# Kernel optimization log

Measured on AMD Instinct MI355X. Metric: run time of the kernel, lower is better.

Reference implementation:

```python
import jax, jax.numpy as jnp
import numpy as np

DIM = 128
HEADS = 4
POS_DIM = (DIM // 4) // 4  # DynamicPosBias: pos_dim = (dim//4)//4 = 8


def _layernorm(x, g, b, eps=1e-5):
    m = x.mean(-1, keepdims=True)
    v = x.var(-1, keepdims=True)
    return (x - m) / jnp.sqrt(v + eps) * g + b


def setup_inputs() -> dict:
    key = jax.random.key(0)
    ks = jax.random.split(key, 16)
    B_, N, C = 64, 512, DIM
    s = 0.02
    inp = {
        "x": jax.random.normal(ks[0], (B_, N, C), jnp.float32),
        "y": jax.random.normal(ks[1], (B_, N, C), jnp.float32),
        "H": 8, "W": 8, "D": 8,
        "qkv_w": jax.random.normal(ks[2], (3 * C, C), jnp.float32) * s,
        "qkv_b": jnp.zeros((3 * C,), jnp.float32),
        "proj_w": jax.random.normal(ks[3], (C, C), jnp.float32) * s,
        "proj_b": jnp.zeros((C,), jnp.float32),
        "pos_proj_w": jax.random.normal(ks[4], (POS_DIM, 3), jnp.float32) * s,
        "pos_proj_b": jnp.zeros((POS_DIM,), jnp.float32),
        "ln1_g": jnp.ones((POS_DIM,), jnp.float32),
        "ln1_b": jnp.zeros((POS_DIM,), jnp.float32),
        "p1_w": jax.random.normal(ks[5], (POS_DIM, POS_DIM), jnp.float32) * s,
        "p1_b": jnp.zeros((POS_DIM,), jnp.float32),
        "ln2_g": jnp.ones((POS_DIM,), jnp.float32),
        "ln2_b": jnp.zeros((POS_DIM,), jnp.float32),
        "p2_w": jax.random.normal(ks[6], (POS_DIM, POS_DIM), jnp.float32) * s,
        "p2_b": jnp.zeros((POS_DIM,), jnp.float32),
        "ln3_g": jnp.ones((POS_DIM,), jnp.float32),
        "ln3_b": jnp.zeros((POS_DIM,), jnp.float32),
        "p3_w": jax.random.normal(ks[7], (HEADS, POS_DIM), jnp.float32) * s,
        "p3_b": jnp.zeros((HEADS,), jnp.float32),
    }
    return inp


def _rel_pos_static(H, W, D):
    # biases table: all relative offsets, shape ((2H-1)(2W-1)(2D-1), 3)
    bh = np.arange(1 - H, H)
    bw = np.arange(1 - W, W)
    bd = np.arange(1 - D, D)
    biases = np.stack(np.meshgrid(bh, bw, bd, indexing="ij")).reshape(3, -1).T
    # relative position index, shape (N, N)
    coords = np.stack(np.meshgrid(np.arange(H), np.arange(W), np.arange(D), indexing="ij")).reshape(3, -1)
    rel = coords[:, :, None] - coords[:, None, :]  # (3, N, N)
    rel = rel.transpose(1, 2, 0).astype(np.int64)
    rel[:, :, 0] += H - 1
    rel[:, :, 1] += W - 1
    rel[:, :, 2] += D - 1
    rel[:, :, 0] *= (2 * W - 1) * (2 * D - 1)
    rel[:, :, 1] *= 2 * D - 1
    idx = rel.sum(-1)  # (N, N)
    return jnp.asarray(biases, jnp.float32), jnp.asarray(idx)


def reference(x, y, H, W, D, qkv_w, qkv_b, proj_w, proj_b,
              pos_proj_w, pos_proj_b, ln1_g, ln1_b, p1_w, p1_b,
              ln2_g, ln2_b, p2_w, p2_b, ln3_g, ln3_b, p3_w, p3_b):
    B_, N, C = x.shape
    h = p3_b.shape[0]
    hd = C // h
    scale = hd ** -0.5

    def qkv_fn(t):
        q3 = (t @ qkv_w.T + qkv_b).reshape(B_, N, 3, h, hd)
        q3 = q3.transpose(2, 0, 3, 1, 4)  # (3, B, h, N, hd)
        return q3[0], q3[1], q3[2]

    q, k, v = qkv_fn(x)
    # NOTE: original code uses self.qkv(y) (not qkv_y) -- reproduced faithfully
    q_y, k_y, v_y = qkv_fn(y)

    attn = jnp.einsum("bhnd,bhmd->bhnm", q * scale, k_y)  # (B, h, N, N)

    biases, idx = _rel_pos_static(H, W, D)
    # DynamicPosBias, residual=False: pos3(pos2(pos1(pos_proj(b))))
    pos = biases @ pos_proj_w.T + pos_proj_b
    pos = jax.nn.relu(_layernorm(pos, ln1_g, ln1_b)) @ p1_w.T + p1_b
    pos = jax.nn.relu(_layernorm(pos, ln2_g, ln2_b)) @ p2_w.T + p2_b
    pos = jax.nn.relu(_layernorm(pos, ln3_g, ln3_b)) @ p3_w.T + p3_b  # (table, h)
    rpb = pos[idx.reshape(-1)].reshape(N, N, h).transpose(2, 0, 1)  # (h, N, N)

    attn = jax.nn.softmax(attn + rpb[None], axis=-1)
    out = jnp.einsum("bhnm,bhmd->bhnd", attn, v_y)
    out = out.transpose(0, 2, 1, 3).reshape(B_, N, C)
    out = out @ proj_w.T + proj_b
    return out
```

## Files before the change

### kernel.cpp

```cpp
#include <hip/hip_runtime.h>
#include <hip/hip_bf16.h>

typedef __attribute__((ext_vector_type(4))) float f32x4;
typedef __attribute__((ext_vector_type(8))) short bf16x8;
typedef __attribute__((ext_vector_type(4))) short bf16x4;
typedef __attribute__((ext_vector_type(2))) unsigned int u32x2;

#define DEV static __device__ __forceinline__

constexpr float LOG2E  = 1.4426950408889634f;
constexpr float QSCALE = 0.17677669529663687f * LOG2E;

constexpr size_t OFF_Q   = 0;
constexpr size_t OFF_K   = (size_t)8  << 20;
constexpr size_t OFF_V   = (size_t)16 << 20;
constexpr size_t OFF_RPB = (size_t)24 << 20;
constexpr size_t OFF_AO  = (size_t)27 << 20;
constexpr size_t OFF_POS = (size_t)35 << 20;
constexpr size_t OFF_WQ  = (size_t)36 << 20;
constexpr size_t OFF_WP  = (size_t)37 << 20;

DEV short f2b(float f) {
  union { __bf16 h; short s; } u;
  u.h = (__bf16)f;
  return u.s;
}
DEV float b2f(unsigned int u) {
  union { unsigned int u; float f; } x; x.u = u; return x.f;
}
DEV unsigned int pkbf(float a, float b) {
  union { __bf16 h; unsigned short s; } ua, ub;
  ua.h = (__bf16)a; ub.h = (__bf16)b;
  return (unsigned int)ua.s | ((unsigned int)ub.s << 16);
}

DEV void ln_relu8(const float* v, const float* __restrict__ g,
                  const float* __restrict__ b, float* t) {
  float m = 0.f;
#pragma unroll
  for (int i = 0; i < 8; i++) m += v[i];
  m *= 0.125f;
  float var = 0.f;
#pragma unroll
  for (int i = 0; i < 8; i++) { float d = v[i] - m; var += d * d; }
  var *= 0.125f;
  float inv = 1.0f / sqrtf(var + 1e-5f);
#pragma unroll
  for (int i = 0; i < 8; i++) {
    float u = (v[i] - m) * inv * g[i] + b[i];
    t[i] = u > 0.f ? u : 0.f;
  }
}

DEV void mm8(const float* t, const float* __restrict__ w,
             const float* __restrict__ c, float* o) {
#pragma unroll
  for (int oo = 0; oo < 8; oo++) {
    float a = c[oo];
#pragma unroll
    for (int i = 0; i < 8; i++) a += t[i] * w[oo * 8 + i];
    o[oo] = a;
  }
}

__global__ void ca_setup(
    const float* __restrict__ qkv_w, const float* __restrict__ proj_w,
    short* __restrict__ wq, short* __restrict__ wp,
    const float* __restrict__ pw, const float* __restrict__ pb,
    const float* __restrict__ g1, const float* __restrict__ b1,
    const float* __restrict__ w1, const float* __restrict__ c1,
    const float* __restrict__ g2, const float* __restrict__ b2,
    const float* __restrict__ w2, const float* __restrict__ c2,
    const float* __restrict__ g3, const float* __restrict__ b3,
    const float* __restrict__ w3, const float* __restrict__ c3,
    float* __restrict__ pos_out) {
  const int blk = blockIdx.x;
  if (blk < 256) {
    int i = blk * 256 + threadIdx.x;
    if (i < 49152) {
      float f = qkv_w[i];
      if (i < 16384) f *= QSCALE;
      wq[i] = f2b(f);
    } else {
      int j = i - 49152;
      wp[j] = f2b(proj_w[j]);
    }
    return;
  }
  int r = (blk - 256) * 256 + threadIdx.x;
  if (r >= 3375) return;
  float x0 = (float)(r / 225 - 7);
  float x1 = (float)((r / 15) % 15 - 7);
  float x2 = (float)(r % 15 - 7);
  float v[8], t[8], u[8];
#pragma unroll
  for (int o = 0; o < 8; o++)
    v[o] = x0 * pw[o * 3] + x1 * pw[o * 3 + 1] + x2 * pw[o * 3 + 2] + pb[o];
  ln_relu8(v, g1, b1, t);
  mm8(t, w1, c1, u);
  ln_relu8(u, g2, b2, t);
  mm8(t, w2, c2, v);
  ln_relu8(v, g3, b3, t);
#pragma unroll
  for (int hh = 0; hh < 4; hh++) {
    float a = c3[hh];
#pragma unroll
    for (int i = 0; i < 8; i++) a += t[i] * w3[hh * 8 + i];
    pos_out[r * 4 + hh] = a * LOG2E;
  }
}

__global__ void ca_rpb(const float* __restrict__ pos, short* __restrict__ rpbf) {
  int gid = blockIdx.x * 256 + threadIdx.x;
  int lane = gid & 63, jc = (gid >> 6) & 31, qg = (gid >> 11) & 31, hh = gid >> 16;
  int q = qg * 16 + (lane & 15);
  int j0 = jc * 16 + (lane >> 4) * 4;
  bf16x4 outv;
#pragma unroll
  for (int r = 0; r < 4; r++) {
    int j = j0 + r;
    int rh = (q >> 6) - (j >> 6) + 7;
    int rw = ((q >> 3) & 7) - ((j >> 3) & 7) + 7;
    int rd = (q & 7) - (j & 7) + 7;
    int idx = (rh * 15 + rw) * 15 + rd;
    outv[r] = f2b(pos[idx * 4 + hh]);
  }
  *(bf16x4*)(rpbf + (size_t)gid * 4) = outv;
}

__global__ __launch_bounds__(256) void ca_qkv(
    const float* __restrict__ x, const float* __restrict__ y,
    const short* __restrict__ wq, const float* __restrict__ qkv_b,
    short* __restrict__ gq, short* __restrict__ gk, short* __restrict__ gv) {
  __shared__ short lds[16384];
  const int z = blockIdx.y;
  const int t0 = blockIdx.x * 64;
  const int b_ = t0 >> 9;
  const int n0 = t0 & 511;
  const int tid = threadIdx.x;
  const float* __restrict__ in = (z == 0) ? x : y;
#pragma unroll
  for (int i = 0; i < 8; i++) {
    int flat = i * 1024 + tid * 4;
    f32x4 f = *(const f32x4*)(in + (size_t)t0 * 128 + flat);
    int row = flat >> 7, col = flat & 127;
    bf16x4 hv;
#pragma unroll
    for (int e = 0; e < 4; e++) hv[e] = f2b(f[e]);
    *(bf16x4*)(lds + row * 136 + col) = hv;
  }
  __syncthreads();
  const int w = tid >> 6, lane = tid & 63, lr = lane & 15, lg = lane >> 4;
  bf16x8 afrag[4];
  {
    const short* ap = lds + (w * 16 + lr) * 136 + lg * 8;
#pragma unroll
    for (int k4 = 0; k4 < 4; k4++) afrag[k4] = *(const bf16x8*)(ap + k4 * 32);
  }
  __syncthreads();

  const int nct = z ? 16 : 8;
  for (int ct = 0; ct < nct; ct++) {
    const int col = z * 128 + ct * 16;
    float bias = qkv_b[col + lr];
    if (z == 0) bias *= QSCALE;
    f32x4 acc = {bias, bias, bias, bias};
    const short* bp = wq + (size_t)(col + lr) * 128 + lg * 8;
#pragma unroll
    for (int k4 = 0; k4 < 4; k4++) {
      bf16x8 bfr = *(const bf16x8*)(bp + k4 * 32);
      acc = __builtin_amdgcn_mfma_f32_16x16x32_bf16(afrag[k4], bfr, acc, 0, 0, 0);
    }
    if (z == 1 && ct >= 8) {
      const int hv_ = (ct - 8) >> 1;
      const int dh = (ct - 8) & 1;
      const int base = 8192 + (((hv_ * 2 + (w >> 1)) * 2 + dh) * 512) + lane * 8 + (w & 1) * 4;
      *(unsigned int*)(lds + base)     = pkbf(acc[0], acc[1]);
      *(unsigned int*)(lds + base + 2) = pkbf(acc[2], acc[3]);
    } else {
      const int d = (ct & 1) * 16 + lr;
      const int base = (w * 4 + (ct >> 1)) * 512 + 128 * (d >> 3) + (d & 7);
#pragma unroll
      for (int r = 0; r < 4; r++)
        lds[base + (lg * 4 + r) * 8] = f2b(acc[r]);
    }
  }
  __syncthreads();
  if (z == 0) {
#pragma unroll
    for (int kk = 0; kk < 4; kk++) {
      const int c = kk * 4 + w, hh = c & 3, tg = c >> 2;
      bf16x8 vd = *(const bf16x8*)(lds + c * 512 + lane * 8);
      *(bf16x8*)(gq + (((size_t)b_ * 4 + hh) * 32 + (n0 >> 4) + tg) * 512 + lane * 8) = vd;
    }
  } else {
#pragma unroll
    for (int kk = 0; kk < 4; kk++) {
      const int c = kk * 4 + w, hh = c & 3, tg = c >> 2;
      bf16x8 vd = *(const bf16x8*)(lds + c * 512 + lane * 8);
      *(bf16x8*)(gk + (((size_t)b_ * 4 + hh) * 32 + (n0 >> 4) + tg) * 512 + lane * 8) = vd;
    }
#pragma unroll
    for (int kk = 0; kk < 4; kk++) {
      const int c = kk * 4 + w, hh = c >> 2, ul = (c >> 1) & 1, dh = c & 1;
      bf16x8 vd = *(const bf16x8*)(lds + 8192 + c * 512 + lane * 8);
      *(bf16x8*)(gv + ((((size_t)b_ * 4 + hh) * 16 + (n0 >> 5) + ul) * 2 + dh) * 512 + lane * 8) = vd;
    }
  }
}

DEV void stage_kv(const short* kg, const short* vg, short* buf, int T, int w, int lane) {
#pragma unroll
  for (int i = 0; i < 4; i++) {
    const int c = w * 4 + i;
    const short* src;
    short* dst;
    if (c < 8) {
      src = kg + ((size_t)(T * 8 + c)) * 512 + lane * 8;
      dst = buf + c * 512;
    } else {
      src = vg + ((size_t)(T * 8 + c - 8)) * 512 + lane * 8;
      dst = buf + 4096 + (c - 8) * 512;
    }
    __builtin_amdgcn_global_load_lds((const __attribute__((address_space(1))) void*)src,
                                     (__attribute__((address_space(3))) void*)dst, 16, 0, 0);
  }
}

__global__ __launch_bounds__(256, 4) void ca_attn(
    const short* __restrict__ qfrag, const short* __restrict__ kfrag,
    const short* __restrict__ vfrag, const short* __restrict__ rpbf,
    short* __restrict__ aob) {
  __shared__ short kv[2][8192];
  const int bid = blockIdx.x;
  const int qt = bid >> 8, rem = bid & 255;
  const int b_ = rem >> 2, hh = rem & 3;
  const int bh = b_ * 4 + hh;
  const int tid = threadIdx.x;
  const int w = tid >> 6, lane = tid & 63, lg = lane >> 4;
  const int q0 = qt * 64 + w * 16, qg = (q0 >> 4);

  const short* kg = kfrag + (size_t)bh * 16384;
  const short* vg = vfrag + (size_t)bh * 16384;
  const bf16x8 qf = *(const bf16x8*)(qfrag + ((size_t)bh * 32 + qg) * 512 + lane * 8);
  const short* bp = rpbf + ((size_t)(hh * 32 + qg) << 13) + lane * 4;

  union PU { bf16x8 v; unsigned int u[4]; };
  PU ones;
  ones.u[0] = 0x3F803F80u; ones.u[1] = 0x3F803F80u;
  ones.u[2] = 0x3F803F80u; ones.u[3] = 0x3F803F80u;

  stage_kv(kg, vg, &kv[0][0], 0, w, lane);
  __syncthreads();

  f32x4 o0 = {0.f, 0.f, 0.f, 0.f}, o1 = {0.f, 0.f, 0.f, 0.f}, o2 = {0.f, 0.f, 0.f, 0.f};

  for (int T = 0; T < 4; T++) {
    const int cur = T & 1;
    if (T < 3) stage_kv(kg, vg, &kv[cur ^ 1][0], T + 1, w, lane);
    const short* kt = &kv[cur][0];
    const short* vt = &kv[cur][4096];

    u32x2 bw[8];
#pragma unroll
    for (int t = 0; t < 8; t++) bw[t] = *(const u32x2*)(bp + (size_t)(T * 8 + t) * 256);

#pragma unroll
    for (int uu = 0; uu < 4; uu++) {
      PU p;
#pragma unroll
      for (int half = 0; half < 2; half++) {
        const int t = uu * 2 + half;
        bf16x8 kf = *(const bf16x8*)(kt + t * 512 + lane * 8);
        f32x4 cin;
        cin[0] = b2f(bw[t].x << 16);
        cin[1] = b2f(bw[t].x & 0xFFFF0000u);
        cin[2] = b2f(bw[t].y << 16);
        cin[3] = b2f(bw[t].y & 0xFFFF0000u);
        f32x4 s = __builtin_amdgcn_mfma_f32_16x16x32_bf16(kf, qf, cin, 0, 0, 0);
        p.u[half * 2 + 0] = pkbf(__builtin_exp2f(s[0]), __builtin_exp2f(s[1]));
        p.u[half * 2 + 1] = pkbf(__builtin_exp2f(s[2]), __builtin_exp2f(s[3]));
      }
      bf16x8 vf0 = *(const bf16x8*)(vt + (uu * 2 + 0) * 512 + lane * 8);
      bf16x8 vf1 = *(const bf16x8*)(vt + (uu * 2 + 1) * 512 + lane * 8);
      o0 = __builtin_amdgcn_mfma_f32_16x16x32_bf16(p.v, vf0, o0, 0, 0, 0);
      o1 = __builtin_amdgcn_mfma_f32_16x16x32_bf16(p.v, vf1, o1, 0, 0, 0);
      o2 = __builtin_amdgcn_mfma_f32_16x16x32_bf16(p.v, ones.v, o2, 0, 0, 0);
    }
    if (T < 3) __syncthreads();
  }

  short* pt = &kv[0][w * 1024];
  const int lr = lane & 15;
#pragma unroll
  for (int r = 0; r < 4; r++) {
    float iv = 1.0f / o2[r];
    pt[(lg * 4 + r) * 40 + lr] = f2b(o0[r] * iv);
    pt[(lg * 4 + r) * 40 + 16 + lr] = f2b(o1[r] * iv);
  }
  asm volatile("s_waitcnt lgkmcnt(0)" ::: "memory");
  __builtin_amdgcn_sched_barrier(0);
  {
    const int qq = lane >> 2, pp = lane & 3;
    bf16x8 od = *(const bf16x8*)(pt + qq * 40 + pp * 8);
    *(bf16x8*)(aob + ((size_t)bh * 512 + q0 + qq) * 32 + pp * 8) = od;
  }
}

__global__ __launch_bounds__(256) void ca_proj(
    const short* __restrict__ aob, const short* __restrict__ wp,
    const float* __restrict__ proj_b, float* __restrict__ out) {
  const int t0 = blockIdx.x * 64;
  const int b_ = t0 >> 9, n0 = t0 & 511;
  const int tid = threadIdx.x;
  const int w = tid >> 6, lane = tid & 63, lr = lane & 15, lg = lane >> 4;
  bf16x8 afrag[4];
#pragma unroll
  for (int k4 = 0; k4 < 4; k4++)
    afrag[k4] = *(const bf16x8*)(aob + (((size_t)b_ * 4 + k4) * 512 + n0 + w * 16 + lr) * 32 + lg * 8);
#pragma unroll
  for (int ct = 0; ct < 8; ct++) {
    float bias = proj_b[ct * 16 + lr];
    f32x4 acc = {bias, bias, bias, bias};
    const short* bp = wp + (size_t)(ct * 16 + lr) * 128 + lg * 8;
#pragma unroll
    for (int k4 = 0; k4 < 4; k4++) {
      bf16x8 bfr = *(const bf16x8*)(bp + k4 * 32);
      acc = __builtin_amdgcn_mfma_f32_16x16x32_bf16(afrag[k4], bfr, acc, 0, 0, 0);
    }
#pragma unroll
    for (int r = 0; r < 4; r++)
      out[(size_t)(t0 + w * 16 + lg * 4 + r) * 128 + ct * 16 + lr] = acc[r];
  }
}

extern "C" void kernel_launch(void* const* d_in, const int* in_sizes, int n_in,
                              void* d_out, int out_size, void* d_ws, size_t ws_size,
                              hipStream_t stream) {
  const float* x      = (const float*)d_in[0];
  const float* y      = (const float*)d_in[1];
  const float* qkv_w  = (const float*)d_in[5];
  const float* qkv_b  = (const float*)d_in[6];
  const float* proj_w = (const float*)d_in[7];
  const float* proj_b = (const float*)d_in[8];
  const float* pos_w  = (const float*)d_in[9];
  const float* pos_b  = (const float*)d_in[10];
  const float* ln1g = (const float*)d_in[11];
  const float* ln1b = (const float*)d_in[12];
  const float* p1w  = (const float*)d_in[13];
  const float* p1b  = (const float*)d_in[14];
  const float* ln2g = (const float*)d_in[15];
  const float* ln2b = (const float*)d_in[16];
  const float* p2w  = (const float*)d_in[17];
  const float* p2b  = (const float*)d_in[18];
  const float* ln3g = (const float*)d_in[19];
  const float* ln3b = (const float*)d_in[20];
  const float* p3w  = (const float*)d_in[21];
  const float* p3b  = (const float*)d_in[22];
  float* out = (float*)d_out;

  char* ws = (char*)d_ws;
  short* gq    = (short*)(ws + OFF_Q);
  short* gk    = (short*)(ws + OFF_K);
  short* gv    = (short*)(ws + OFF_V);
  short* rpbf  = (short*)(ws + OFF_RPB);
  short* aob   = (short*)(ws + OFF_AO);
  float* posb  = (float*)(ws + OFF_POS);
  short* wq    = (short*)(ws + OFF_WQ);
  short* wp    = (short*)(ws + OFF_WP);

  ca_setup<<<270, 256, 0, stream>>>(qkv_w, proj_w, wq, wp,
                                    pos_w, pos_b, ln1g, ln1b, p1w, p1b,
                                    ln2g, ln2b, p2w, p2b, ln3g, ln3b, p3w, p3b, posb);
  ca_rpb<<<1024, 256, 0, stream>>>(posb, rpbf);
  ca_qkv<<<dim3(512, 2), 256, 0, stream>>>(x, y, wq, qkv_b, gq, gk, gv);
  ca_attn<<<2048, 256, 0, stream>>>(gq, gk, gv, rpbf, aob);
  ca_proj<<<512, 256, 0, stream>>>(aob, wp, proj_b, out);
}
```

Measured before the change: 84.36 us.

## Fuse pos-bias setup with RPB gather, widen blocks, stage full K/V once

Merges the pos-bias MLP and relative-position-bias gather into one kernel that keeps each head's table in LDS, dropping one launch and a global round trip. QKV, attention and projection kernels move to 512-thread blocks covering 128 tokens. Attention now loads all of K/V for a (batch, head) into LDS once instead of double-buffering four tiles, and raises wave priority around the PV MFMAs. The projection output is staged through LDS so the fp32 global stores are coalesced. These changes trade a larger LDS footprint per block for fewer launches and fewer barriers, which may lower occupancy.

```diff
diff --git a/kernel.cpp b/kernel.cpp
--- a/kernel.cpp
+++ b/kernel.cpp
@@ -16,7 +16,6 @@
 constexpr size_t OFF_V   = (size_t)16 << 20;
 constexpr size_t OFF_RPB = (size_t)24 << 20;
 constexpr size_t OFF_AO  = (size_t)27 << 20;
-constexpr size_t OFF_POS = (size_t)35 << 20;
 constexpr size_t OFF_WQ  = (size_t)36 << 20;
 constexpr size_t OFF_WP  = (size_t)37 << 20;
 
@@ -63,85 +62,84 @@
   }
 }
 
-__global__ void ca_setup(
+__global__ void ca_pre(
     const float* __restrict__ qkv_w, const float* __restrict__ proj_w,
     short* __restrict__ wq, short* __restrict__ wp,
+    short* __restrict__ rpbf,
     const float* __restrict__ pw, const float* __restrict__ pb,
     const float* __restrict__ g1, const float* __restrict__ b1,
     const float* __restrict__ w1, const float* __restrict__ c1,
     const float* __restrict__ g2, const float* __restrict__ b2,
     const float* __restrict__ w2, const float* __restrict__ c2,
     const float* __restrict__ g3, const float* __restrict__ b3,
-    const float* __restrict__ w3, const float* __restrict__ c3,
-    float* __restrict__ pos_out) {
+    const float* __restrict__ w3, const float* __restrict__ c3) {
   const int blk = blockIdx.x;
-  if (blk < 256) {
-    int i = blk * 256 + threadIdx.x;
+  if (blk >= 256) {
+    int i = (blk - 256) * 256 + threadIdx.x;
     if (i < 49152) {
       float f = qkv_w[i];
       if (i < 16384) f *= QSCALE;
       wq[i] = f2b(f);
     } else {
-      int j = i - 49152;
-      wp[j] = f2b(proj_w[j]);
+      wp[i - 49152] = f2b(proj_w[i - 49152]);
     }
     return;
   }
-  int r = (blk - 256) * 256 + threadIdx.x;
-  if (r >= 3375) return;
-  float x0 = (float)(r / 225 - 7);
-  float x1 = (float)((r / 15) % 15 - 7);
-  float x2 = (float)(r % 15 - 7);
-  float v[8], t[8], u[8];
-#pragma unroll
-  for (int o = 0; o < 8; o++)
-    v[o] = x0 * pw[o * 3] + x1 * pw[o * 3 + 1] + x2 * pw[o * 3 + 2] + pb[o];
-  ln_relu8(v, g1, b1, t);
-  mm8(t, w1, c1, u);
-  ln_relu8(u, g2, b2, t);
-  mm8(t, w2, c2, v);
-  ln_relu8(v, g3, b3, t);
-#pragma unroll
-  for (int hh = 0; hh < 4; hh++) {
+  __shared__ float plds[3375];
+  const int hh = blk >> 6;
+  for (int r = threadIdx.x; r < 3375; r += 256) {
+    float x0 = (float)(r / 225 - 7);
+    float x1 = (float)((r / 15) % 15 - 7);
+    float x2 = (float)(r % 15 - 7);
+    float v[8], t[8], u[8];
+#pragma unroll
+    for (int o = 0; o < 8; o++)
+      v[o] = x0 * pw[o * 3] + x1 * pw[o * 3 + 1] + x2 * pw[o * 3 + 2] + pb[o];
+    ln_relu8(v, g1, b1, t);
+    mm8(t, w1, c1, u);
+    ln_relu8(u, g2, b2, t);
+    mm8(t, w2, c2, v);
+    ln_relu8(v, g3, b3, t);
     float a = c3[hh];
 #pragma unroll
     for (int i = 0; i < 8; i++) a += t[i] * w3[hh * 8 + i];
-    pos_out[r * 4 + hh] = a * LOG2E;
-  }
-}
-
-__global__ void ca_rpb(const float* __restrict__ pos, short* __restrict__ rpbf) {
-  int gid = blockIdx.x * 256 + threadIdx.x;
-  int lane = gid & 63, jc = (gid >> 6) & 31, qg = (gid >> 11) & 31, hh = gid >> 16;
-  int q = qg * 16 + (lane & 15);
-  int j0 = jc * 16 + (lane >> 4) * 4;
-  bf16x4 outv;
-#pragma unroll
-  for (int r = 0; r < 4; r++) {
-    int j = j0 + r;
-    int rh = (q >> 6) - (j >> 6) + 7;
-    int rw = ((q >> 3) & 7) - ((j >> 3) & 7) + 7;
-    int rd = (q & 7) - (j & 7) + 7;
-    int idx = (rh * 15 + rw) * 15 + rd;
-    outv[r] = f2b(pos[idx * 4 + hh]);
-  }
-  *(bf16x4*)(rpbf + (size_t)gid * 4) = outv;
-}
-
-__global__ __launch_bounds__(256) void ca_qkv(
+    plds[r] = a * LOG2E;
+  }
+  __syncthreads();
+#pragma unroll
+  for (int k = 0; k < 4; k++) {
+    int gid = (hh << 16) + (blk & 63) * 1024 + k * 256 + (int)threadIdx.x;
+    int lane = gid & 63, jc = (gid >> 6) & 31, qg = (gid >> 11) & 31;
+    int q = qg * 16 + (lane & 15);
+    int j0 = jc * 16 + (lane >> 4) * 4;
+    bf16x4 outv;
+#pragma unroll
+    for (int r = 0; r < 4; r++) {
+      int j = j0 + r;
+      int rh = (q >> 6) - (j >> 6) + 7;
+      int rw = ((q >> 3) & 7) - ((j >> 3) & 7) + 7;
+      int rd = (q & 7) - (j & 7) + 7;
+      int idx = (rh * 15 + rw) * 15 + rd;
+      outv[r] = f2b(plds[idx]);
+    }
+    *(bf16x4*)(rpbf + (size_t)gid * 4) = outv;
+  }
+}
+
+__global__ __launch_bounds__(512) void ca_qkv(
     const float* __restrict__ x, const float* __restrict__ y,
     const short* __restrict__ wq, const float* __restrict__ qkv_b,
     short* __restrict__ gq, short* __restrict__ gk, short* __restrict__ gv) {
-  __shared__ short lds[16384];
+  __shared__ short lds[32768];
   const int z = blockIdx.y;
-  const int t0 = blockIdx.x * 64;
+  const int t0 = blockIdx.x * 128;
   const int b_ = t0 >> 9;
   const int n0 = t0 & 511;
   const int tid = threadIdx.x;
   const float* __restrict__ in = (z == 0) ? x : y;
 #pragma unroll
   for (int i = 0; i < 8; i++) {
-    int flat = i * 1024 + tid * 4;
+    int flat = i * 2048 + tid * 4;
     f32x4 f = *(const f32x4*)(in + (size_t)t0 * 128 + flat);
     int row = flat >> 7, col = flat & 127;
     bf16x4 hv;
@@ -159,139 +157,145 @@
   }
   __syncthreads();
 
-  const int nct = z ? 16 : 8;
-  for (int ct = 0; ct < nct; ct++) {
-    const int col = z * 128 + ct * 16;
-    float bias = qkv_b[col + lr];
-    if (z == 0) bias *= QSCALE;
-    f32x4 acc = {bias, bias, bias, bias};
-    const short* bp = wq + (size_t)(col + lr) * 128 + lg * 8;
-#pragma unroll
-    for (int k4 = 0; k4 < 4; k4++) {
-      bf16x8 bfr = *(const bf16x8*)(bp + k4 * 32);
-      acc = __builtin_amdgcn_mfma_f32_16x16x32_bf16(afrag[k4], bfr, acc, 0, 0, 0);
-    }
-    if (z == 1 && ct >= 8) {
-      const int hv_ = (ct - 8) >> 1;
-      const int dh = (ct - 8) & 1;
-      const int base = 8192 + (((hv_ * 2 + (w >> 1)) * 2 + dh) * 512) + lane * 8 + (w & 1) * 4;
-      *(unsigned int*)(lds + base)     = pkbf(acc[0], acc[1]);
-      *(unsigned int*)(lds + base + 2) = pkbf(acc[2], acc[3]);
-    } else {
+  if (z == 0) {
+#pragma unroll
+    for (int ct = 0; ct < 8; ct++) {
+      const int col = ct * 16;
+      float bias = qkv_b[col + lr] * QSCALE;
+      f32x4 acc = {bias, bias, bias, bias};
+      const short* bp = wq + (size_t)(col + lr) * 128 + lg * 8;
+#pragma unroll
+      for (int k4 = 0; k4 < 4; k4++) {
+        bf16x8 bfr = *(const bf16x8*)(bp + k4 * 32);
+        acc = __builtin_amdgcn_mfma_f32_16x16x32_bf16(afrag[k4], bfr, acc, 0, 0, 0);
+      }
       const int d = (ct & 1) * 16 + lr;
       const int base = (w * 4 + (ct >> 1)) * 512 + 128 * (d >> 3) + (d & 7);
 #pragma unroll
       for (int r = 0; r < 4; r++)
         lds[base + (lg * 4 + r) * 8] = f2b(acc[r]);
     }
+  } else {
+#pragma unroll
+    for (int ct = 0; ct < 16; ct++) {
+      const int col = 128 + ct * 16;
+      float bias = qkv_b[col + lr];
+      f32x4 acc = {bias, bias, bias, bias};
+      const short* bp = wq + (size_t)(col + lr) * 128 + lg * 8;
+#pragma unroll
+      for (int k4 = 0; k4 < 4; k4++) {
+        bf16x8 bfr = *(const bf16x8*)(bp + k4 * 32);
+        acc = __builtin_amdgcn_mfma_f32_16x16x32_bf16(afrag[k4], bfr, acc, 0, 0, 0);
+      }
+      if (ct >= 8) {
+        const int hv_ = (ct - 8) >> 1;
+        const int dh = (ct - 8) & 1;
+        const int base = 16384 + ((hv_ * 8 + (w >> 1) * 2 + dh) * 512) + lane * 8 + (w & 1) * 4;
+        *(unsigned int*)(lds + base)     = pkbf(acc[0], acc[1]);
+        *(unsigned int*)(lds + base + 2) = pkbf(acc[2], acc[3]);
+      } else {
+        const int d = (ct & 1) * 16 + lr;
+        const int base = (w * 4 + (ct >> 1)) * 512 + 128 * (d >> 3) + (d & 7);
+#pragma unroll
+        for (int r = 0; r < 4; r++)
+          lds[base + (lg * 4 + r) * 8] = f2b(acc[r]);
+      }
+    }
   }
   __syncthreads();
   if (z == 0) {
 #pragma unroll
     for (int kk = 0; kk < 4; kk++) {
-      const int c = kk * 4 + w, hh = c & 3, tg = c >> 2;
+      const int c = kk * 8 + w, hh = c & 3, tg = c >> 2;
       bf16x8 vd = *(const bf16x8*)(lds + c * 512 + lane * 8);
       *(bf16x8*)(gq + (((size_t)b_ * 4 + hh) * 32 + (n0 >> 4) + tg) * 512 + lane * 8) = vd;
     }
   } else {
 #pragma unroll
-    for (int kk = 0; kk < 4; kk++) {
-      const int c = kk * 4 + w, hh = c & 3, tg = c >> 2;
+    for (int kk = 0; kk < 8; kk++) {
+      const int c = kk * 8 + w;
       bf16x8 vd = *(const bf16x8*)(lds + c * 512 + lane * 8);
-      *(bf16x8*)(gk + (((size_t)b_ * 4 + hh) * 32 + (n0 >> 4) + tg) * 512 + lane * 8) = vd;
-    }
-#pragma unroll
-    for (int kk = 0; kk < 4; kk++) {
-      const int c = kk * 4 + w, hh = c >> 2, ul = (c >> 1) & 1, dh = c & 1;
-      bf16x8 vd = *(const bf16x8*)(lds + 8192 + c * 512 + lane * 8);
-      *(bf16x8*)(gv + ((((size_t)b_ * 4 + hh) * 16 + (n0 >> 5) + ul) * 2 + dh) * 512 + lane * 8) = vd;
-    }
-  }
-}
-
-DEV void stage_kv(const short* kg, const short* vg, short* buf, int T, int w, int lane) {
-#pragma unroll
-  for (int i = 0; i < 4; i++) {
-    const int c = w * 4 + i;
-    const short* src;
-    short* dst;
-    if (c < 8) {
-      src = kg + ((size_t)(T * 8 + c)) * 512 + lane * 8;
-      dst = buf + c * 512;
-    } else {
-      src = vg + ((size_t)(T * 8 + c - 8)) * 512 + lane * 8;
-      dst = buf + 4096 + (c - 8) * 512;
-    }
-    __builtin_amdgcn_global_load_lds((const __attribute__((address_space(1))) void*)src,
-                                     (__attribute__((address_space(3))) void*)dst, 16, 0, 0);
-  }
-}
-
-__global__ __launch_bounds__(256, 4) void ca_attn(
+      if (c < 32) {
+        const int hh = c & 3, tg = c >> 2;
+        *(bf16x8*)(gk + (((size_t)b_ * 4 + hh) * 32 + (n0 >> 4) + tg) * 512 + lane * 8) = vd;
+      } else {
+        const int cv = c - 32, dh = cv & 1, ul = (cv >> 1) & 3, hh = cv >> 3;
+        *(bf16x8*)(gv + ((((size_t)b_ * 4 + hh) * 16 + (n0 >> 5) + ul) * 2 + dh) * 512 + lane * 8) = vd;
+      }
+    }
+  }
+}
+
+__global__ __launch_bounds__(512, 4) void ca_attn(
     const short* __restrict__ qfrag, const short* __restrict__ kfrag,
     const short* __restrict__ vfrag, const short* __restrict__ rpbf,
     short* __restrict__ aob) {
-  __shared__ short kv[2][8192];
+  __shared__ short lds[37888];
   const int bid = blockIdx.x;
-  const int qt = bid >> 8, rem = bid & 255;
+  const int qb = bid >> 8, rem = bid & 255;
   const int b_ = rem >> 2, hh = rem & 3;
   const int bh = b_ * 4 + hh;
   const int tid = threadIdx.x;
-  const int w = tid >> 6, lane = tid & 63, lg = lane >> 4;
-  const int q0 = qt * 64 + w * 16, qg = (q0 >> 4);
+  const int w = tid >> 6, lane = tid & 63, lg = lane >> 4, lr = lane & 15;
+  const int qg = qb * 8 + w;
+  const int q0 = qg * 16;
 
   const short* kg = kfrag + (size_t)bh * 16384;
   const short* vg = vfrag + (size_t)bh * 16384;
   const bf16x8 qf = *(const bf16x8*)(qfrag + ((size_t)bh * 32 + qg) * 512 + lane * 8);
   const short* bp = rpbf + ((size_t)(hh * 32 + qg) << 13) + lane * 4;
 
+#pragma unroll
+  for (int i = 0; i < 8; i++) {
+    const int c = w * 8 + i;
+    const short* src = (c < 32) ? (kg + (size_t)c * 512 + lane * 8)
+                                : (vg + (size_t)(c - 32) * 512 + lane * 8);
+    __builtin_amdgcn_global_load_lds((const __attribute__((address_space(1))) void*)src,
+                                     (__attribute__((address_space(3))) void*)(lds + c * 512), 16, 0, 0);
+  }
+  __syncthreads();
+
+  const short* kt = lds;
+  const short* vt = lds + 16384;
   union PU { bf16x8 v; unsigned int u[4]; };
   PU ones;
   ones.u[0] = 0x3F803F80u; ones.u[1] = 0x3F803F80u;
   ones.u[2] = 0x3F803F80u; ones.u[3] = 0x3F803F80u;
 
-  stage_kv(kg, vg, &kv[0][0], 0, w, lane);
-  __syncthreads();
-
   f32x4 o0 = {0.f, 0.f, 0.f, 0.f}, o1 = {0.f, 0.f, 0.f, 0.f}, o2 = {0.f, 0.f, 0.f, 0.f};
 
-  for (int T = 0; T < 4; T++) {
-    const int cur = T & 1;
-    if (T < 3) stage_kv(kg, vg, &kv[cur ^ 1][0], T + 1, w, lane);
-    const short* kt = &kv[cur][0];
-    const short* vt = &kv[cur][4096];
-
-    u32x2 bw[8];
-#pragma unroll
-    for (int t = 0; t < 8; t++) bw[t] = *(const u32x2*)(bp + (size_t)(T * 8 + t) * 256);
-
-#pragma unroll
-    for (int uu = 0; uu < 4; uu++) {
-      PU p;
-#pragma unroll
-      for (int half = 0; half < 2; half++) {
-        const int t = uu * 2 + half;
-        bf16x8 kf = *(const bf16x8*)(kt + t * 512 + lane * 8);
-        f32x4 cin;
-        cin[0] = b2f(bw[t].x << 16);
-        cin[1] = b2f(bw[t].x & 0xFFFF0000u);
-        cin[2] = b2f(bw[t].y << 16);
-        cin[3] = b2f(bw[t].y & 0xFFFF0000u);
-        f32x4 s = __builtin_amdgcn_mfma_f32_16x16x32_bf16(kf, qf, cin, 0, 0, 0);
-        p.u[half * 2 + 0] = pkbf(__builtin_exp2f(s[0]), __builtin_exp2f(s[1]));
-        p.u[half * 2 + 1] = pkbf(__builtin_exp2f(s[2]), __builtin_exp2f(s[3]));
-      }
-      bf16x8 vf0 = *(const bf16x8*)(vt + (uu * 2 + 0) * 512 + lane * 8);
-      bf16x8 vf1 = *(const bf16x8*)(vt + (uu * 2 + 1) * 512 + lane * 8);
-      o0 = __builtin_amdgcn_mfma_f32_16x16x32_bf16(p.v, vf0, o0, 0, 0, 0);
-      o1 = __builtin_amdgcn_mfma_f32_16x16x32_bf16(p.v, vf1, o1, 0, 0, 0);
-      o2 = __builtin_amdgcn_mfma_f32_16x16x32_bf16(p.v, ones.v, o2, 0, 0, 0);
-    }
-    if (T < 3) __syncthreads();
-  }
-
-  short* pt = &kv[0][w * 1024];
-  const int lr = lane & 15;
+#pragma unroll 4
+  for (int tp = 0; tp < 16; tp++) {
+    u32x2 bw0 = *(const u32x2*)(bp + (size_t)(2 * tp + 0) * 256);
+    u32x2 bw1 = *(const u32x2*)(bp + (size_t)(2 * tp + 1) * 256);
+    bf16x8 kf0 = *(const bf16x8*)(kt + (2 * tp + 0) * 512 + lane * 8);
+    bf16x8 kf1 = *(const bf16x8*)(kt + (2 * tp + 1) * 512 + lane * 8);
+    f32x4 c0, c1;
+    c0[0] = b2f(bw0.x << 16);
+    c0[1] = b2f(bw0.x & 0xFFFF0000u);
+    c0[2] = b2f(bw0.y << 16);
+    c0[3] = b2f(bw0.y & 0xFFFF0000u);
+    c1[0] = b2f(bw1.x << 16);
+    c1[1] = b2f(bw1.x & 0xFFFF0000u);
+    c1[2] = b2f(bw1.y << 16);
+    c1[3] = b2f(bw1.y & 0xFFFF0000u);
+    f32x4 s0 = __builtin_amdgcn_mfma_f32_16x16x32_bf16(kf0, qf, c0, 0, 0, 0);
+    f32x4 s1 = __builtin_amdgcn_mfma_f32_16x16x32_bf16(kf1, qf, c1, 0, 0, 0);
+    PU p;
+    p.u[0] = pkbf(__builtin_exp2f(s0[0]), __builtin_exp2f(s0[1]));
+    p.u[1] = pkbf(__builtin_exp2f(s0[2]), __builtin_exp2f(s0[3]));
+    p.u[2] = pkbf(__builtin_exp2f(s1[0]), __builtin_exp2f(s1[1]));
+    p.u[3] = pkbf(__builtin_exp2f(s1[2]), __builtin_exp2f(s1[3]));
+    bf16x8 vf0 = *(const bf16x8*)(vt + (tp * 2 + 0) * 512 + lane * 8);
+    bf16x8 vf1 = *(const bf16x8*)(vt + (tp * 2 + 1) * 512 + lane * 8);
+    __builtin_amdgcn_s_setprio(1);
+    o0 = __builtin_amdgcn_mfma_f32_16x16x32_bf16(p.v, vf0, o0, 0, 0, 0);
+    o1 = __builtin_amdgcn_mfma_f32_16x16x32_bf16(p.v, vf1, o1, 0, 0, 0);
+    o2 = __builtin_amdgcn_mfma_f32_16x16x32_bf16(p.v, ones.v, o2, 0, 0, 0);
+    __builtin_amdgcn_s_setprio(0);
+  }
+
+  short* pt = lds + 32768 + w * 640;
 #pragma unroll
   for (int r = 0; r < 4; r++) {
     float iv = 1.0f / o2[r];
@@ -307,10 +311,11 @@
   }
 }
 
-__global__ __launch_bounds__(256) void ca_proj(
+__global__ __launch_bounds__(512) void ca_proj(
     const short* __restrict__ aob, const short* __restrict__ wp,
     const float* __restrict__ proj_b, float* __restrict__ out) {
-  const int t0 = blockIdx.x * 64;
+  __shared__ float plds[16896];
+  const int t0 = blockIdx.x * 128;
   const int b_ = t0 >> 9, n0 = t0 & 511;
   const int tid = threadIdx.x;
   const int w = tid >> 6, lane = tid & 63, lr = lane & 15, lg = lane >> 4;
@@ -318,6 +323,7 @@
 #pragma unroll
   for (int k4 = 0; k4 < 4; k4++)
     afrag[k4] = *(const bf16x8*)(aob + (((size_t)b_ * 4 + k4) * 512 + n0 + w * 16 + lr) * 32 + lg * 8);
+  float* pt = plds + w * 2112;
 #pragma unroll
   for (int ct = 0; ct < 8; ct++) {
     float bias = proj_b[ct * 16 + lr];
@@ -330,7 +336,16 @@
     }
 #pragma unroll
     for (int r = 0; r < 4; r++)
-      out[(size_t)(t0 + w * 16 + lg * 4 + r) * 128 + ct * 16 + lr] = acc[r];
+      pt[(lg * 4 + r) * 132 + ct * 16 + lr] = acc[r];
+  }
+  asm volatile("s_waitcnt lgkmcnt(0)" ::: "memory");
+  __builtin_amdgcn_sched_barrier(0);
+#pragma unroll
+  for (int i = 0; i < 8; i++) {
+    int f = i * 256 + lane * 4;
+    int row = f >> 7, col = f & 127;
+    f32x4 v = *(const f32x4*)(pt + row * 132 + col);
+    *(f32x4*)(out + (size_t)(t0 + w * 16) * 128 + f) = v;
   }
 }
 
@@ -365,15 +380,13 @@
   short* gv    = (short*)(ws + OFF_V);
   short* rpbf  = (short*)(ws + OFF_RPB);
   short* aob   = (short*)(ws + OFF_AO);
-  float* posb  = (float*)(ws + OFF_POS);
   short* wq    = (short*)(ws + OFF_WQ);
   short* wp    = (short*)(ws + OFF_WP);
 
-  ca_setup<<<270, 256, 0, stream>>>(qkv_w, proj_w, wq, wp,
-                                    pos_w, pos_b, ln1g, ln1b, p1w, p1b,
-                                    ln2g, ln2b, p2w, p2b, ln3g, ln3b, p3w, p3b, posb);
-  ca_rpb<<<1024, 256, 0, stream>>>(posb, rpbf);
-  ca_qkv<<<dim3(512, 2), 256, 0, stream>>>(x, y, wq, qkv_b, gq, gk, gv);
-  ca_attn<<<2048, 256, 0, stream>>>(gq, gk, gv, rpbf, aob);
-  ca_proj<<<512, 256, 0, stream>>>(aob, wp, proj_b, out);
-}
+  ca_pre<<<512, 256, 0, stream>>>(qkv_w, proj_w, wq, wp, rpbf,
+                                  pos_w, pos_b, ln1g, ln1b, p1w, p1b,
+                                  ln2g, ln2b, p2w, p2b, ln3g, ln3b, p3w, p3b);
+  ca_qkv<<<dim3(256, 2), 512, 0, stream>>>(x, y, wq, qkv_b, gq, gk, gv);
+  ca_attn<<<1024, 512, 0, stream>>>(gq, gk, gv, rpbf, aob);
+  ca_proj<<<256, 512, 0, stream>>>(aob, wp, proj_b, out);
+}
```

Result: slower. 96.91 us (+14.9%).
